# Kernel tuning notes

Hardware: AMD Instinct MI355X
Metric: run time of the kernel (lower is better)

Reference implementation:

```python
import jax, jax.numpy as jnp
import numpy as np

NUM_USERS = 100000
NUM_ITEMS = 50000
EMBED_DIM = 64
NUM_LAYERS = 3
NUM_EDGES = 1250000
N = NUM_USERS + NUM_ITEMS


def setup_inputs() -> dict:
    key = jax.random.key(0)
    k1, k2, k3 = jax.random.split(key, 3)
    edge_index = jax.random.randint(k1, (2, NUM_EDGES), 0, N, dtype=jnp.int64)
    # nn.init.normal_(std=0.1)
    user_weight = 0.1 * jax.random.normal(k2, (NUM_USERS, EMBED_DIM), dtype=jnp.float32)
    item_weight = 0.1 * jax.random.normal(k3, (NUM_ITEMS, EMBED_DIM), dtype=jnp.float32)
    return {"edge_index": edge_index, "user_weight": user_weight, "item_weight": item_weight}


def reference(edge_index, user_weight, item_weight):
    src = edge_index[0]  # [E]
    dst = edge_index[1]  # [E]
    # degrees counted from dst column only (matches the torch loop)
    deg = jax.ops.segment_sum(jnp.ones_like(src, dtype=jnp.float32), dst, num_segments=N)
    norm = 1.0 / (jnp.sqrt(deg[src]) * jnp.sqrt(deg[dst]))  # [E]
    norm = jnp.where(jnp.isfinite(norm), norm, 0.0)

    emb = jnp.concatenate([user_weight, item_weight], axis=0)  # [N, D]
    acc = emb  # running sum over layer outputs (incl. layer 0)
    cur = emb
    for _ in range(NUM_LAYERS):
        msgs = cur[src] * norm[:, None]  # [E, D]
        cur = jax.ops.segment_sum(msgs, dst, num_segments=N)
        acc = acc + cur
    all_embeddings = acc / (NUM_LAYERS + 1)
    user_embeddings = all_embeddings[:NUM_USERS]
    item_embeddings = all_embeddings[NUM_USERS:]
    return all_embeddings, user_embeddings, item_embeddings
```

## Files before the change

### kernel.cpp

```cpp
#include <hip/hip_runtime.h>


#define NU 100000
#define NI 50000
#define NN 150000
#define HALF 75000
#define DIM 64
#define NE 1250000
#define NF (NN * DIM)
#define NF4 (NF / 4)
#define SLOT 40
#define NBK 293
#define BSTRIDE 5120
#define PB 256
#define EPB ((NE + PB - 1) / PB)

typedef unsigned short ushort_t;

__device__ inline ushort_t f2bf(float f) {
    unsigned u = __float_as_uint(f);
    return (ushort_t)((u + 0x7FFF + ((u >> 16) & 1)) >> 16);
}
__device__ inline float bflo(unsigned u) { return __uint_as_float(u << 16); }
__device__ inline float bfhi(unsigned u) { return __uint_as_float(u & 0xffff0000u); }

__global__ void __launch_bounds__(1024) phaseA_kernel(const int* __restrict__ src,
                                                      const int* __restrict__ dst,
                                                      int* __restrict__ bcursor,
                                                      int* __restrict__ part) {
    __shared__ int hist[NBK];
    __shared__ int cur[NBK];
    int b = blockIdx.x;
    int tid = threadIdx.x;
    if (tid < NBK) hist[tid] = 0;
    __syncthreads();
    int e0 = b * EPB;
    int e1 = min(e0 + EPB, NE);
    for (int e = e0 + tid; e < e1; e += 1024)
        atomicAdd(&hist[dst[e] >> 9], 1);
    __syncthreads();
    if (tid < NBK) {
        int h = hist[tid];
        int base = h ? atomicAdd(&bcursor[tid], h) : 0;
        cur[tid] = tid * BSTRIDE + base;
    }
    __syncthreads();
    for (int e = e0 + tid; e < e1; e += 1024) {
        int dd = dst[e];
        int s = src[e];
        int p = atomicAdd(&cur[dd >> 9], 1);
        part[p] = ((dd & 511) << 18) | s;
    }
}

__global__ void __launch_bounds__(1024) phaseB_kernel(const int* __restrict__ bcursor,
                                                      const int* __restrict__ part,
                                                      int* __restrict__ cursor,
                                                      float* __restrict__ rdeg,
                                                      int* __restrict__ slots,
                                                      const float4* __restrict__ uw4,
                                                      const float4* __restrict__ iw4,
                                                      ushort_t* __restrict__ embb) {
    __shared__ int dcount[512];
    __shared__ float rfs[512];
    int b = blockIdx.x;
    int tid = threadIdx.x;
    int cnt = min(bcursor[b], BSTRIDE);
    int nodebase = b * 512;
    if (tid < 512) dcount[tid] = 0;
    __syncthreads();
    const int* pb = part + b * BSTRIDE;
    for (int i = tid; i < cnt; i += 1024) {
        int v = pb[i];
        int dloc = v >> 18;
        int p = atomicAdd(&dcount[dloc], 1);
        if (p < SLOT)
            slots[(nodebase + dloc) * SLOT + p] = v & 0x3FFFF;
    }
    __syncthreads();
    if (tid < 512) {
        int n = nodebase + tid;
        float r = 0.0f;
        if (n < NN) {
            int c = min(dcount[tid], SLOT);
            cursor[n] = c;
            r = (c > 0) ? rsqrtf((float)c) : 0.0f;
            rdeg[n] = r;
            int e = (c <= 8) ? 8 : ((c + 7) & ~7);
            for (int k = c; k < e; k++)
                slots[n * SLOT + k] = NN;
        }
        rfs[tid] = r;
    }
    __syncthreads();
    int nnode = min(512, NN - nodebase);
    int lim = nnode * 16;
    for (int q = tid; q < lim; q += 1024) {
        int nl = q >> 4;
        int node = nodebase + nl;
        int c4 = q & 15;
        float4 v = (node < NU) ? uw4[node * 16 + c4] : iw4[(node - NU) * 16 + c4];
        float r = rfs[nl];
        ushort4 h;
        h.x = f2bf(v.x * r); h.y = f2bf(v.y * r);
        h.z = f2bf(v.z * r); h.w = f2bf(v.w * r);
        *(ushort4*)(embb + node * DIM + c4 * 4) = h;
    }
}

template <int LAYER>
__global__ void __launch_bounds__(1024) gather_kernel(const int* __restrict__ cursor,
                                                      const float* __restrict__ rdeg,
                                                      const int* __restrict__ slots,
                                                      const ushort_t* __restrict__ cur,
                                                      const float4* __restrict__ uw4,
                                                      const float4* __restrict__ iw4,
                                                      float4* __restrict__ acc,
                                                      ushort_t* __restrict__ nxt) {
    int wid = blockIdx.x * 16 + (threadIdx.x >> 6);
    int n0 = __builtin_amdgcn_readfirstlane(wid);
    if (n0 >= HALF) return;
    int n1 = n0 + HALF;
    int lane = threadIdx.x & 63;
    int j = lane >> 4;
    int d = lane & 15;
    bool j1 = (j & 1) != 0;
    bool j2 = (j & 2) != 0;
    int dg0 = __builtin_amdgcn_readfirstlane(cursor[n0]);
    int dg1 = __builtin_amdgcn_readfirstlane(cursor[n1]);
    float rd0 = __uint_as_float(__builtin_amdgcn_readfirstlane(__float_as_uint(rdeg[n0])));
    float rd1 = __uint_as_float(__builtin_amdgcn_readfirstlane(__float_as_uint(rdeg[n1])));
    const int* sb0 = slots + n0 * SLOT;
    const int* sb1 = slots + n1 * SLOT;
    float a0 = 0, a1 = 0, a2 = 0, a3 = 0;
    float b0 = 0, b1 = 0, b2 = 0, b3 = 0;

#define GRP(SB, C, X0, X1, X2, X3)                                             \
    {                                                                          \
        int4 qa = *(const int4*)((SB) + (C));                                  \
        int4 qb = *(const int4*)((SB) + (C) + 4);                              \
        int ta = j1 ? qa.y : qa.x;                                             \
        int tb = j1 ? qa.w : qa.z;                                             \
        int sva = j2 ? tb : ta;                                                \
        int tc = j1 ? qb.y : qb.x;                                             \
        int td = j1 ? qb.w : qb.z;                                             \
        int svb = j2 ? td : tc;                                                \
        uint2 ua = *((const uint2*)(cur + sva * DIM) + d);                     \
        uint2 ub = *((const uint2*)(cur + svb * DIM) + d);                     \
        X0 += bflo(ua.x); X1 += bfhi(ua.x);                                    \
        X2 += bflo(ua.y); X3 += bfhi(ua.y);                                    \
        X0 += bflo(ub.x); X1 += bfhi(ub.x);                                    \
        X2 += bflo(ub.y); X3 += bfhi(ub.y);                                    \
    }

    GRP(sb0, 0, a0, a1, a2, a3)
    GRP(sb1, 0, b0, b1, b2, b3)
    for (int c = 8; c < dg0; c += 8) GRP(sb0, c, a0, a1, a2, a3)
    for (int c = 8; c < dg1; c += 8) GRP(sb1, c, b0, b1, b2, b3)
#undef GRP

    a0 += __shfl_xor(a0, 16); a1 += __shfl_xor(a1, 16);
    a2 += __shfl_xor(a2, 16); a3 += __shfl_xor(a3, 16);
    b0 += __shfl_xor(b0, 16); b1 += __shfl_xor(b1, 16);
    b2 += __shfl_xor(b2, 16); b3 += __shfl_xor(b3, 16);
    a0 += __shfl_xor(a0, 32); a1 += __shfl_xor(a1, 32);
    a2 += __shfl_xor(a2, 32); a3 += __shfl_xor(a3, 32);
    b0 += __shfl_xor(b0, 32); b1 += __shfl_xor(b1, 32);
    b2 += __shfl_xor(b2, 32); b3 += __shfl_xor(b3, 32);

    float c00 = rd0 * a0, c01 = rd0 * a1, c02 = rd0 * a2, c03 = rd0 * a3;
    float c10 = rd1 * b0, c11 = rd1 * b1, c12 = rd1 * b2, c13 = rd1 * b3;

    if (j == 0) {
        int i0 = n0 * 16 + d;
        int i1 = n1 * 16 + d;
        if (LAYER == 1) {
            float4 e0 = uw4[n0 * 16 + d];
            float4 e1 = (n1 < NU) ? uw4[n1 * 16 + d] : iw4[(n1 - NU) * 16 + d];
            acc[i0] = make_float4(e0.x + c00, e0.y + c01, e0.z + c02, e0.w + c03);
            acc[i1] = make_float4(e1.x + c10, e1.y + c11, e1.z + c12, e1.w + c13);
            ushort4 h0, h1;
            h0.x = f2bf(rd0 * c00); h0.y = f2bf(rd0 * c01);
            h0.z = f2bf(rd0 * c02); h0.w = f2bf(rd0 * c03);
            h1.x = f2bf(rd1 * c10); h1.y = f2bf(rd1 * c11);
            h1.z = f2bf(rd1 * c12); h1.w = f2bf(rd1 * c13);
            *(ushort4*)(nxt + n0 * DIM + d * 4) = h0;
            *(ushort4*)(nxt + n1 * DIM + d * 4) = h1;
        } else if (LAYER == 2) {
            float4 t0 = acc[i0];
            float4 t1 = acc[i1];
            acc[i0] = make_float4(t0.x + c00, t0.y + c01, t0.z + c02, t0.w + c03);
            acc[i1] = make_float4(t1.x + c10, t1.y + c11, t1.z + c12, t1.w + c13);
            ushort4 h0, h1;
            h0.x = f2bf(rd0 * c00); h0.y = f2bf(rd0 * c01);
            h0.z = f2bf(rd0 * c02); h0.w = f2bf(rd0 * c03);
            h1.x = f2bf(rd1 * c10); h1.y = f2bf(rd1 * c11);
            h1.z = f2bf(rd1 * c12); h1.w = f2bf(rd1 * c13);
            *(ushort4*)(nxt + n0 * DIM + d * 4) = h0;
            *(ushort4*)(nxt + n1 * DIM + d * 4) = h1;
        } else {
            float4 t0 = acc[i0];
            float4 t1 = acc[i1];
            float4 v0 = make_float4((t0.x + c00) * 0.25f, (t0.y + c01) * 0.25f,
                                    (t0.z + c02) * 0.25f, (t0.w + c03) * 0.25f);
            float4 v1 = make_float4((t1.x + c10) * 0.25f, (t1.y + c11) * 0.25f,
                                    (t1.z + c12) * 0.25f, (t1.w + c13) * 0.25f);
            acc[i0] = v0;
            acc[NF4 + i0] = v0;
            acc[i1] = v1;
            acc[NF4 + i1] = v1;
        }
    }
}

extern "C" void kernel_launch(void* const* d_in, const int* in_sizes, int n_in,
                              void* d_out, int out_size, void* d_ws, size_t ws_size,
                              hipStream_t stream) {
    const int* edge = (const int*)d_in[0];
    const int* src = edge;
    const int* dst = edge + NE;
    const float* uw = (const float*)d_in[1];
    const float* iw = (const float*)d_in[2];
    float* out = (float*)d_out;

    int* cursor    = (int*)d_ws;
    float* rdeg    = (float*)(cursor + NN);
    int* bcursor   = (int*)(rdeg + NN);
    int* slots     = bcursor + 320;
    int* part      = slots + NN * SLOT;
    ushort_t* embb = (ushort_t*)(part + NBK * BSTRIDE);
    ushort_t* bufA = embb;
    ushort_t* bufT = (ushort_t*)(out + NF);

    hipMemsetAsync(bcursor, 0, NBK * sizeof(int), stream);
    hipMemsetAsync(embb + NF, 0, DIM * sizeof(ushort_t), stream);
    hipMemsetAsync(bufT + NF, 0, DIM * sizeof(ushort_t), stream);

    phaseA_kernel<<<PB, 1024, 0, stream>>>(src, dst, bcursor, part);
    phaseB_kernel<<<NBK, 1024, 0, stream>>>(bcursor, part, cursor, rdeg, slots,
                                            (const float4*)uw, (const float4*)iw, embb);

    const int GB = (HALF + 15) / 16;

    gather_kernel<1><<<GB, 1024, 0, stream>>>(cursor, rdeg, slots, embb,
                                              (const float4*)uw, (const float4*)iw,
                                              (float4*)out, bufT);
    gather_kernel<2><<<GB, 1024, 0, stream>>>(cursor, rdeg, slots, bufT,
                                              (const float4*)uw, (const float4*)iw,
                                              (float4*)out, bufA);
    gather_kernel<3><<<GB, 1024, 0, stream>>>(cursor, rdeg, slots, bufA,
                                              (const float4*)uw, (const float4*)iw,
                                              (float4*)out, nullptr);
}
```

Baseline: 284.2 us.

## Compact CSR slot layout with per-node offsets and four nodes per wave

Replaces the fixed 40-slot-per-node adjacency array with a compact per-bucket CSR built by a shared-memory prefix scan in phaseB, and stores each node's offset and degree as an int2. The gather kernel now processes four nodes per wave instead of two, with each lane reading a pair of neighbor indices directly instead of selecting from int4 loads. The two memsets for the sentinel rows are folded into phaseB. This shrinks slot-array traffic and raises memory-level parallelism per wave, at the cost of more registers and a longer phaseB with extra syncs. It also drops the 40-neighbor cap, so degree handling becomes exact.

```diff
diff --git a/kernel.cpp b/kernel.cpp
--- a/kernel.cpp
+++ b/kernel.cpp
@@ -4,14 +4,14 @@
 #define NU 100000
 #define NI 50000
 #define NN 150000
-#define HALF 75000
+#define QUARTER 37500
 #define DIM 64
 #define NE 1250000
 #define NF (NN * DIM)
 #define NF4 (NF / 4)
-#define SLOT 40
 #define NBK 293
 #define BSTRIDE 5120
+#define BSLOT 8192
 #define PB 256
 #define EPB ((NE + PB - 1) / PB)
 
@@ -55,44 +55,76 @@
 
 __global__ void __launch_bounds__(1024) phaseB_kernel(const int* __restrict__ bcursor,
                                                       const int* __restrict__ part,
-                                                      int* __restrict__ cursor,
+                                                      int2* __restrict__ od,
                                                       float* __restrict__ rdeg,
                                                       int* __restrict__ slots,
                                                       const float4* __restrict__ uw4,
                                                       const float4* __restrict__ iw4,
-                                                      ushort_t* __restrict__ embb) {
+                                                      ushort_t* __restrict__ embb,
+                                                      ushort_t* __restrict__ bufT) {
+    __shared__ int stash[BSTRIDE];
     __shared__ int dcount[512];
+    __shared__ int cnt2[512];
+    __shared__ int sc[512];
+    __shared__ int offL[512];
     __shared__ float rfs[512];
     int b = blockIdx.x;
     int tid = threadIdx.x;
     int cnt = min(bcursor[b], BSTRIDE);
     int nodebase = b * 512;
     if (tid < 512) dcount[tid] = 0;
+    if (b == 0 && tid < DIM) {
+        embb[NF + tid] = 0;
+        bufT[NF + tid] = 0;
+    }
     __syncthreads();
     const int* pb = part + b * BSTRIDE;
     for (int i = tid; i < cnt; i += 1024) {
         int v = pb[i];
-        int dloc = v >> 18;
-        int p = atomicAdd(&dcount[dloc], 1);
-        if (p < SLOT)
-            slots[(nodebase + dloc) * SLOT + p] = v & 0x3FFFF;
+        stash[i] = v;
+        atomicAdd(&dcount[v >> 18], 1);
     }
     __syncthreads();
     if (tid < 512) {
+        int c = dcount[tid];
+        int pad = (c <= 8) ? 8 : ((c + 7) & ~7);
+        sc[tid] = pad;
         int n = nodebase + tid;
         float r = 0.0f;
         if (n < NN) {
-            int c = min(dcount[tid], SLOT);
-            cursor[n] = c;
             r = (c > 0) ? rsqrtf((float)c) : 0.0f;
             rdeg[n] = r;
-            int e = (c <= 8) ? 8 : ((c + 7) & ~7);
-            for (int k = c; k < e; k++)
-                slots[n * SLOT + k] = NN;
         }
         rfs[tid] = r;
     }
     __syncthreads();
+    for (int ofs = 1; ofs < 512; ofs <<= 1) {
+        int v = 0;
+        if (tid < 512 && tid >= ofs) v = sc[tid - ofs];
+        __syncthreads();
+        if (tid < 512 && tid >= ofs) sc[tid] += v;
+        __syncthreads();
+    }
+    if (tid < 512) {
+        int c = dcount[tid];
+        int pad = (c <= 8) ? 8 : ((c + 7) & ~7);
+        int off = b * BSLOT + sc[tid] - pad;
+        offL[tid] = off;
+        cnt2[tid] = 0;
+        int n = nodebase + tid;
+        if (n < NN) {
+            od[n] = make_int2(off, c);
+            for (int k = c; k < pad; k++)
+                slots[off + k] = NN;
+        }
+    }
+    __syncthreads();
+    for (int i = tid; i < cnt; i += 1024) {
+        int v = stash[i];
+        int dloc = v >> 18;
+        int p = atomicAdd(&cnt2[dloc], 1);
+        slots[offL[dloc] + p] = v & 0x3FFFF;
+    }
     int nnode = min(512, NN - nodebase);
     int lim = nnode * 16;
     for (int q = tid; q < lim; q += 1024) {
@@ -109,7 +141,7 @@
 }
 
 template <int LAYER>
-__global__ void __launch_bounds__(1024) gather_kernel(const int* __restrict__ cursor,
+__global__ void __launch_bounds__(1024) gather_kernel(const int2* __restrict__ od,
                                                       const float* __restrict__ rdeg,
                                                       const int* __restrict__ slots,
                                                       const ushort_t* __restrict__ cur,
@@ -119,98 +151,113 @@
                                                       ushort_t* __restrict__ nxt) {
     int wid = blockIdx.x * 16 + (threadIdx.x >> 6);
     int n0 = __builtin_amdgcn_readfirstlane(wid);
-    if (n0 >= HALF) return;
-    int n1 = n0 + HALF;
+    if (n0 >= QUARTER) return;
+    int n1 = n0 + QUARTER;
+    int n2 = n0 + 2 * QUARTER;
+    int n3 = n0 + 3 * QUARTER;
     int lane = threadIdx.x & 63;
-    int j = lane >> 4;
+    int j2 = (lane >> 3) & ~1;
     int d = lane & 15;
-    bool j1 = (j & 1) != 0;
-    bool j2 = (j & 2) != 0;
-    int dg0 = __builtin_amdgcn_readfirstlane(cursor[n0]);
-    int dg1 = __builtin_amdgcn_readfirstlane(cursor[n1]);
+
+    int2 v0 = od[n0];
+    int2 v1 = od[n1];
+    int2 v2 = od[n2];
+    int2 v3 = od[n3];
+    int of0 = __builtin_amdgcn_readfirstlane(v0.x);
+    int dg0 = __builtin_amdgcn_readfirstlane(v0.y);
+    int of1 = __builtin_amdgcn_readfirstlane(v1.x);
+    int dg1 = __builtin_amdgcn_readfirstlane(v1.y);
+    int of2 = __builtin_amdgcn_readfirstlane(v2.x);
+    int dg2 = __builtin_amdgcn_readfirstlane(v2.y);
+    int of3 = __builtin_amdgcn_readfirstlane(v3.x);
+    int dg3 = __builtin_amdgcn_readfirstlane(v3.y);
     float rd0 = __uint_as_float(__builtin_amdgcn_readfirstlane(__float_as_uint(rdeg[n0])));
     float rd1 = __uint_as_float(__builtin_amdgcn_readfirstlane(__float_as_uint(rdeg[n1])));
-    const int* sb0 = slots + n0 * SLOT;
-    const int* sb1 = slots + n1 * SLOT;
-    float a0 = 0, a1 = 0, a2 = 0, a3 = 0;
-    float b0 = 0, b1 = 0, b2 = 0, b3 = 0;
+    float rd2 = __uint_as_float(__builtin_amdgcn_readfirstlane(__float_as_uint(rdeg[n2])));
+    float rd3 = __uint_as_float(__builtin_amdgcn_readfirstlane(__float_as_uint(rdeg[n3])));
+    const int* sb0 = slots + of0;
+    const int* sb1 = slots + of1;
+    const int* sb2 = slots + of2;
+    const int* sb3 = slots + of3;
+    float x0 = 0, x1 = 0, x2 = 0, x3 = 0;
+    float y0 = 0, y1 = 0, y2 = 0, y3 = 0;
+    float z0 = 0, z1 = 0, z2 = 0, z3 = 0;
+    float w0 = 0, w1 = 0, w2 = 0, w3 = 0;
 
 #define GRP(SB, C, X0, X1, X2, X3)                                             \
     {                                                                          \
-        int4 qa = *(const int4*)((SB) + (C));                                  \
-        int4 qb = *(const int4*)((SB) + (C) + 4);                              \
-        int ta = j1 ? qa.y : qa.x;                                             \
-        int tb = j1 ? qa.w : qa.z;                                             \
-        int sva = j2 ? tb : ta;                                                \
-        int tc = j1 ? qb.y : qb.x;                                             \
-        int td = j1 ? qb.w : qb.z;                                             \
-        int svb = j2 ? td : tc;                                                \
-        uint2 ua = *((const uint2*)(cur + sva * DIM) + d);                     \
-        uint2 ub = *((const uint2*)(cur + svb * DIM) + d);                     \
+        int2 sv = *(const int2*)((SB) + (C) + j2);                             \
+        uint2 ua = *((const uint2*)(cur + sv.x * DIM) + d);                    \
+        uint2 ub = *((const uint2*)(cur + sv.y * DIM) + d);                    \
         X0 += bflo(ua.x); X1 += bfhi(ua.x);                                    \
         X2 += bflo(ua.y); X3 += bfhi(ua.y);                                    \
         X0 += bflo(ub.x); X1 += bfhi(ub.x);                                    \
         X2 += bflo(ub.y); X3 += bfhi(ub.y);                                    \
     }
 
-    GRP(sb0, 0, a0, a1, a2, a3)
-    GRP(sb1, 0, b0, b1, b2, b3)
-    for (int c = 8; c < dg0; c += 8) GRP(sb0, c, a0, a1, a2, a3)
-    for (int c = 8; c < dg1; c += 8) GRP(sb1, c, b0, b1, b2, b3)
+    GRP(sb0, 0, x0, x1, x2, x3)
+    GRP(sb1, 0, y0, y1, y2, y3)
+    GRP(sb2, 0, z0, z1, z2, z3)
+    GRP(sb3, 0, w0, w1, w2, w3)
+    for (int c = 8; c < dg0; c += 8) GRP(sb0, c, x0, x1, x2, x3)
+    for (int c = 8; c < dg1; c += 8) GRP(sb1, c, y0, y1, y2, y3)
+    for (int c = 8; c < dg2; c += 8) GRP(sb2, c, z0, z1, z2, z3)
+    for (int c = 8; c < dg3; c += 8) GRP(sb3, c, w0, w1, w2, w3)
 #undef GRP
 
-    a0 += __shfl_xor(a0, 16); a1 += __shfl_xor(a1, 16);
-    a2 += __shfl_xor(a2, 16); a3 += __shfl_xor(a3, 16);
-    b0 += __shfl_xor(b0, 16); b1 += __shfl_xor(b1, 16);
-    b2 += __shfl_xor(b2, 16); b3 += __shfl_xor(b3, 16);
-    a0 += __shfl_xor(a0, 32); a1 += __shfl_xor(a1, 32);
-    a2 += __shfl_xor(a2, 32); a3 += __shfl_xor(a3, 32);
-    b0 += __shfl_xor(b0, 32); b1 += __shfl_xor(b1, 32);
-    b2 += __shfl_xor(b2, 32); b3 += __shfl_xor(b3, 32);
-
-    float c00 = rd0 * a0, c01 = rd0 * a1, c02 = rd0 * a2, c03 = rd0 * a3;
-    float c10 = rd1 * b0, c11 = rd1 * b1, c12 = rd1 * b2, c13 = rd1 * b3;
-
-    if (j == 0) {
-        int i0 = n0 * 16 + d;
-        int i1 = n1 * 16 + d;
-        if (LAYER == 1) {
-            float4 e0 = uw4[n0 * 16 + d];
-            float4 e1 = (n1 < NU) ? uw4[n1 * 16 + d] : iw4[(n1 - NU) * 16 + d];
-            acc[i0] = make_float4(e0.x + c00, e0.y + c01, e0.z + c02, e0.w + c03);
-            acc[i1] = make_float4(e1.x + c10, e1.y + c11, e1.z + c12, e1.w + c13);
-            ushort4 h0, h1;
-            h0.x = f2bf(rd0 * c00); h0.y = f2bf(rd0 * c01);
-            h0.z = f2bf(rd0 * c02); h0.w = f2bf(rd0 * c03);
-            h1.x = f2bf(rd1 * c10); h1.y = f2bf(rd1 * c11);
-            h1.z = f2bf(rd1 * c12); h1.w = f2bf(rd1 * c13);
-            *(ushort4*)(nxt + n0 * DIM + d * 4) = h0;
-            *(ushort4*)(nxt + n1 * DIM + d * 4) = h1;
-        } else if (LAYER == 2) {
-            float4 t0 = acc[i0];
-            float4 t1 = acc[i1];
-            acc[i0] = make_float4(t0.x + c00, t0.y + c01, t0.z + c02, t0.w + c03);
-            acc[i1] = make_float4(t1.x + c10, t1.y + c11, t1.z + c12, t1.w + c13);
-            ushort4 h0, h1;
-            h0.x = f2bf(rd0 * c00); h0.y = f2bf(rd0 * c01);
-            h0.z = f2bf(rd0 * c02); h0.w = f2bf(rd0 * c03);
-            h1.x = f2bf(rd1 * c10); h1.y = f2bf(rd1 * c11);
-            h1.z = f2bf(rd1 * c12); h1.w = f2bf(rd1 * c13);
-            *(ushort4*)(nxt + n0 * DIM + d * 4) = h0;
-            *(ushort4*)(nxt + n1 * DIM + d * 4) = h1;
-        } else {
-            float4 t0 = acc[i0];
-            float4 t1 = acc[i1];
-            float4 v0 = make_float4((t0.x + c00) * 0.25f, (t0.y + c01) * 0.25f,
-                                    (t0.z + c02) * 0.25f, (t0.w + c03) * 0.25f);
-            float4 v1 = make_float4((t1.x + c10) * 0.25f, (t1.y + c11) * 0.25f,
-                                    (t1.z + c12) * 0.25f, (t1.w + c13) * 0.25f);
-            acc[i0] = v0;
-            acc[NF4 + i0] = v0;
-            acc[i1] = v1;
-            acc[NF4 + i1] = v1;
-        }
-    }
+    x0 += __shfl_xor(x0, 16); x1 += __shfl_xor(x1, 16);
+    x2 += __shfl_xor(x2, 16); x3 += __shfl_xor(x3, 16);
+    y0 += __shfl_xor(y0, 16); y1 += __shfl_xor(y1, 16);
+    y2 += __shfl_xor(y2, 16); y3 += __shfl_xor(y3, 16);
+    z0 += __shfl_xor(z0, 16); z1 += __shfl_xor(z1, 16);
+    z2 += __shfl_xor(z2, 16); z3 += __shfl_xor(z3, 16);
+    w0 += __shfl_xor(w0, 16); w1 += __shfl_xor(w1, 16);
+    w2 += __shfl_xor(w2, 16); w3 += __shfl_xor(w3, 16);
+    x0 += __shfl_xor(x0, 32); x1 += __shfl_xor(x1, 32);
+    x2 += __shfl_xor(x2, 32); x3 += __shfl_xor(x3, 32);
+    y0 += __shfl_xor(y0, 32); y1 += __shfl_xor(y1, 32);
+    y2 += __shfl_xor(y2, 32); y3 += __shfl_xor(y3, 32);
+    z0 += __shfl_xor(z0, 32); z1 += __shfl_xor(z1, 32);
+    z2 += __shfl_xor(z2, 32); z3 += __shfl_xor(z3, 32);
+    w0 += __shfl_xor(w0, 32); w1 += __shfl_xor(w1, 32);
+    w2 += __shfl_xor(w2, 32); w3 += __shfl_xor(w3, 32);
+
+    if ((lane >> 4) != 0) return;
+
+#define EPI(N, RD, A0, A1, A2, A3, EMB)                                        \
+    {                                                                          \
+        float c0 = (RD) * (A0), c1 = (RD) * (A1);                              \
+        float c2 = (RD) * (A2), c3 = (RD) * (A3);                              \
+        int i4 = (N) * 16 + d;                                                 \
+        if (LAYER == 1) {                                                      \
+            float4 e = (EMB);                                                  \
+            acc[i4] = make_float4(e.x + c0, e.y + c1, e.z + c2, e.w + c3);     \
+            ushort4 h;                                                         \
+            h.x = f2bf((RD) * c0); h.y = f2bf((RD) * c1);                      \
+            h.z = f2bf((RD) * c2); h.w = f2bf((RD) * c3);                      \
+            *(ushort4*)(nxt + (N) * DIM + d * 4) = h;                          \
+        } else if (LAYER == 2) {                                               \
+            float4 t = acc[i4];                                                \
+            acc[i4] = make_float4(t.x + c0, t.y + c1, t.z + c2, t.w + c3);     \
+            ushort4 h;                                                         \
+            h.x = f2bf((RD) * c0); h.y = f2bf((RD) * c1);                      \
+            h.z = f2bf((RD) * c2); h.w = f2bf((RD) * c3);                      \
+            *(ushort4*)(nxt + (N) * DIM + d * 4) = h;                          \
+        } else {                                                               \
+            float4 t = acc[i4];                                                \
+            float4 v = make_float4((t.x + c0) * 0.25f, (t.y + c1) * 0.25f,     \
+                                   (t.z + c2) * 0.25f, (t.w + c3) * 0.25f);    \
+            acc[i4] = v;                                                       \
+            acc[NF4 + i4] = v;                                                 \
+        }                                                                      \
+    }
+
+    EPI(n0, rd0, x0, x1, x2, x3, uw4[n0 * 16 + d])
+    EPI(n1, rd1, y0, y1, y2, y3, uw4[n1 * 16 + d])
+    EPI(n2, rd2, z0, z1, z2, z3,
+        ((n2 < NU) ? uw4[n2 * 16 + d] : iw4[(n2 - NU) * 16 + d]))
+    EPI(n3, rd3, w0, w1, w2, w3, iw4[(n3 - NU) * 16 + d])
+#undef EPI
 }
 
 extern "C" void kernel_launch(void* const* d_in, const int* in_sizes, int n_in,
@@ -223,32 +270,31 @@
     const float* iw = (const float*)d_in[2];
     float* out = (float*)d_out;
 
-    int* cursor    = (int*)d_ws;
-    float* rdeg    = (float*)(cursor + NN);
+    int2* od       = (int2*)d_ws;
+    float* rdeg    = (float*)(od + NN);
     int* bcursor   = (int*)(rdeg + NN);
     int* slots     = bcursor + 320;
-    int* part      = slots + NN * SLOT;
+    int* part      = slots + NBK * BSLOT;
     ushort_t* embb = (ushort_t*)(part + NBK * BSTRIDE);
     ushort_t* bufA = embb;
     ushort_t* bufT = (ushort_t*)(out + NF);
 
     hipMemsetAsync(bcursor, 0, NBK * sizeof(int), stream);
-    hipMemsetAsync(embb + NF, 0, DIM * sizeof(ushort_t), stream);
-    hipMemsetAsync(bufT + NF, 0, DIM * sizeof(ushort_t), stream);
 
     phaseA_kernel<<<PB, 1024, 0, stream>>>(src, dst, bcursor, part);
-    phaseB_kernel<<<NBK, 1024, 0, stream>>>(bcursor, part, cursor, rdeg, slots,
-                                            (const float4*)uw, (const float4*)iw, embb);
-
-    const int GB = (HALF + 15) / 16;
-
-    gather_kernel<1><<<GB, 1024, 0, stream>>>(cursor, rdeg, slots, embb,
+    phaseB_kernel<<<NBK, 1024, 0, stream>>>(bcursor, part, od, rdeg, slots,
+                                            (const float4*)uw, (const float4*)iw,
+                                            embb, bufT);
+
+    const int GB = (QUARTER + 15) / 16;
+
+    gather_kernel<1><<<GB, 1024, 0, stream>>>(od, rdeg, slots, embb,
                                               (const float4*)uw, (const float4*)iw,
                                               (float4*)out, bufT);
-    gather_kernel<2><<<GB, 1024, 0, stream>>>(cursor, rdeg, slots, bufT,
+    gather_kernel<2><<<GB, 1024, 0, stream>>>(od, rdeg, slots, bufT,
                                               (const float4*)uw, (const float4*)iw,
                                               (float4*)out, bufA);
-    gather_kernel<3><<<GB, 1024, 0, stream>>>(cursor, rdeg, slots, bufA,
+    gather_kernel<3><<<GB, 1024, 0, stream>>>(od, rdeg, slots, bufA,
                                               (const float4*)uw, (const float4*)iw,
                                               (float4*)out, nullptr);
 }
```

After: 318.2 us. 12.0% more time.

## Replace fixed-slot adjacency with compact CSR-like per-bucket packed slots

Applied to the files above, without the earlier changes.

Phase B now stashes each bucket's edges in shared memory, counts degrees, and runs a prefix scan over padded counts. It then writes neighbour lists contiguously per bucket instead of into fixed 40-entry slots per node, and stores offset and degree packed in one word. The gather kernel recomputes rsqrt from the degree, so it drops the separate cursor and rdeg loads. This shrinks the adjacency footprint and improves locality of slot reads, and it also removes the 40-neighbour truncation. Two small memsets are folded into the kernel, at the cost of extra shared memory and barriers in phase B.

```diff
diff --git a/kernel.cpp b/kernel.cpp
--- a/kernel.cpp
+++ b/kernel.cpp
@@ -9,9 +9,9 @@
 #define NE 1250000
 #define NF (NN * DIM)
 #define NF4 (NF / 4)
-#define SLOT 40
 #define NBK 293
 #define BSTRIDE 5120
+#define BSLOT 8192
 #define PB 256
 #define EPB ((NE + PB - 1) / PB)
 
@@ -55,44 +55,69 @@
 
 __global__ void __launch_bounds__(1024) phaseB_kernel(const int* __restrict__ bcursor,
                                                       const int* __restrict__ part,
-                                                      int* __restrict__ cursor,
-                                                      float* __restrict__ rdeg,
+                                                      unsigned* __restrict__ od,
                                                       int* __restrict__ slots,
                                                       const float4* __restrict__ uw4,
                                                       const float4* __restrict__ iw4,
-                                                      ushort_t* __restrict__ embb) {
+                                                      ushort_t* __restrict__ embb,
+                                                      ushort_t* __restrict__ bufT) {
+    __shared__ int stash[BSTRIDE];
     __shared__ int dcount[512];
+    __shared__ int cnt2[512];
+    __shared__ int sc[512];
+    __shared__ int offL[512];
     __shared__ float rfs[512];
     int b = blockIdx.x;
     int tid = threadIdx.x;
     int cnt = min(bcursor[b], BSTRIDE);
     int nodebase = b * 512;
     if (tid < 512) dcount[tid] = 0;
+    if (b == 0 && tid < DIM) {
+        embb[NF + tid] = 0;
+        bufT[NF + tid] = 0;
+    }
     __syncthreads();
     const int* pb = part + b * BSTRIDE;
     for (int i = tid; i < cnt; i += 1024) {
         int v = pb[i];
+        stash[i] = v;
+        atomicAdd(&dcount[v >> 18], 1);
+    }
+    __syncthreads();
+    if (tid < 512) {
+        int c = dcount[tid];
+        int pad = (c <= 8) ? 8 : ((c + 7) & ~7);
+        sc[tid] = pad;
+        rfs[tid] = (c > 0) ? rsqrtf((float)c) : 0.0f;
+    }
+    __syncthreads();
+    for (int ofs = 1; ofs < 512; ofs <<= 1) {
+        int v = 0;
+        if (tid < 512 && tid >= ofs) v = sc[tid - ofs];
+        __syncthreads();
+        if (tid < 512 && tid >= ofs) sc[tid] += v;
+        __syncthreads();
+    }
+    if (tid < 512) {
+        int c = dcount[tid];
+        int pad = (c <= 8) ? 8 : ((c + 7) & ~7);
+        int off = b * BSLOT + sc[tid] - pad;
+        offL[tid] = off;
+        cnt2[tid] = 0;
+        int n = nodebase + tid;
+        if (n < NN) {
+            od[n] = (unsigned)off | ((unsigned)c << 26);
+            for (int k = c; k < pad; k++)
+                slots[off + k] = NN;
+        }
+    }
+    __syncthreads();
+    for (int i = tid; i < cnt; i += 1024) {
+        int v = stash[i];
         int dloc = v >> 18;
-        int p = atomicAdd(&dcount[dloc], 1);
-        if (p < SLOT)
-            slots[(nodebase + dloc) * SLOT + p] = v & 0x3FFFF;
-    }
-    __syncthreads();
-    if (tid < 512) {
-        int n = nodebase + tid;
-        float r = 0.0f;
-        if (n < NN) {
-            int c = min(dcount[tid], SLOT);
-            cursor[n] = c;
-            r = (c > 0) ? rsqrtf((float)c) : 0.0f;
-            rdeg[n] = r;
-            int e = (c <= 8) ? 8 : ((c + 7) & ~7);
-            for (int k = c; k < e; k++)
-                slots[n * SLOT + k] = NN;
-        }
-        rfs[tid] = r;
-    }
-    __syncthreads();
+        int p = atomicAdd(&cnt2[dloc], 1);
+        slots[offL[dloc] + p] = v & 0x3FFFF;
+    }
     int nnode = min(512, NN - nodebase);
     int lim = nnode * 16;
     for (int q = tid; q < lim; q += 1024) {
@@ -109,8 +134,7 @@
 }
 
 template <int LAYER>
-__global__ void __launch_bounds__(1024) gather_kernel(const int* __restrict__ cursor,
-                                                      const float* __restrict__ rdeg,
+__global__ void __launch_bounds__(1024) gather_kernel(const unsigned* __restrict__ od,
                                                       const int* __restrict__ slots,
                                                       const ushort_t* __restrict__ cur,
                                                       const float4* __restrict__ uw4,
@@ -126,12 +150,16 @@
     int d = lane & 15;
     bool j1 = (j & 1) != 0;
     bool j2 = (j & 2) != 0;
-    int dg0 = __builtin_amdgcn_readfirstlane(cursor[n0]);
-    int dg1 = __builtin_amdgcn_readfirstlane(cursor[n1]);
-    float rd0 = __uint_as_float(__builtin_amdgcn_readfirstlane(__float_as_uint(rdeg[n0])));
-    float rd1 = __uint_as_float(__builtin_amdgcn_readfirstlane(__float_as_uint(rdeg[n1])));
-    const int* sb0 = slots + n0 * SLOT;
-    const int* sb1 = slots + n1 * SLOT;
+    unsigned v0 = (unsigned)__builtin_amdgcn_readfirstlane((int)od[n0]);
+    unsigned v1 = (unsigned)__builtin_amdgcn_readfirstlane((int)od[n1]);
+    int of0 = (int)(v0 & 0x3FFFFFFu);
+    int dg0 = (int)(v0 >> 26);
+    int of1 = (int)(v1 & 0x3FFFFFFu);
+    int dg1 = (int)(v1 >> 26);
+    float rd0 = (dg0 > 0) ? rsqrtf((float)dg0) : 0.0f;
+    float rd1 = (dg1 > 0) ? rsqrtf((float)dg1) : 0.0f;
+    const int* sb0 = slots + of0;
+    const int* sb1 = slots + of1;
     float a0 = 0, a1 = 0, a2 = 0, a3 = 0;
     float b0 = 0, b1 = 0, b2 = 0, b3 = 0;
 
@@ -223,32 +251,30 @@
     const float* iw = (const float*)d_in[2];
     float* out = (float*)d_out;
 
-    int* cursor    = (int*)d_ws;
-    float* rdeg    = (float*)(cursor + NN);
-    int* bcursor   = (int*)(rdeg + NN);
+    unsigned* od   = (unsigned*)d_ws;
+    int* bcursor   = (int*)(od + NN);
     int* slots     = bcursor + 320;
-    int* part      = slots + NN * SLOT;
+    int* part      = slots + NBK * BSLOT;
     ushort_t* embb = (ushort_t*)(part + NBK * BSTRIDE);
     ushort_t* bufA = embb;
     ushort_t* bufT = (ushort_t*)(out + NF);
 
     hipMemsetAsync(bcursor, 0, NBK * sizeof(int), stream);
-    hipMemsetAsync(embb + NF, 0, DIM * sizeof(ushort_t), stream);
-    hipMemsetAsync(bufT + NF, 0, DIM * sizeof(ushort_t), stream);
 
     phaseA_kernel<<<PB, 1024, 0, stream>>>(src, dst, bcursor, part);
-    phaseB_kernel<<<NBK, 1024, 0, stream>>>(bcursor, part, cursor, rdeg, slots,
-                                            (const float4*)uw, (const float4*)iw, embb);
+    phaseB_kernel<<<NBK, 1024, 0, stream>>>(bcursor, part, od, slots,
+                                            (const float4*)uw, (const float4*)iw,
+                                            embb, bufT);
 
     const int GB = (HALF + 15) / 16;
 
-    gather_kernel<1><<<GB, 1024, 0, stream>>>(cursor, rdeg, slots, embb,
+    gather_kernel<1><<<GB, 1024, 0, stream>>>(od, slots, embb,
                                               (const float4*)uw, (const float4*)iw,
                                               (float4*)out, bufT);
-    gather_kernel<2><<<GB, 1024, 0, stream>>>(cursor, rdeg, slots, bufT,
+    gather_kernel<2><<<GB, 1024, 0, stream>>>(od, slots, bufT,
                                               (const float4*)uw, (const float4*)iw,
                                               (float4*)out, bufA);
-    gather_kernel<3><<<GB, 1024, 0, stream>>>(cursor, rdeg, slots, bufA,
+    gather_kernel<3><<<GB, 1024, 0, stream>>>(od, slots, bufA,
                                               (const float4*)uw, (const float4*)iw,
                                               (float4*)out, nullptr);
 }
```

Measured after the change: 307.2 us. +8.1%, slower.

## Fuse three gather layers into a persistent kernel with LDS accumulators

Applied to the files above, without the earlier changes.

The three per-layer gather launches become one persistent kernel of 256 blocks. Each block owns 586 nodes, keeps their fp32 running sums in shared memory, and separates layers with a software grid barrier. This removes the global-memory read-modify-write of the accumulator and two kernel launches. In exchange, occupancy drops to 16 waves per CU for a latency-bound gather, and the barrier assumes every block is resident at once. Separately, the partition kernel now stages packed edges in shared memory so src and dst are read only once, and it uses twice as many blocks.

```diff
diff --git a/kernel.cpp b/kernel.cpp
--- a/kernel.cpp
+++ b/kernel.cpp
@@ -4,7 +4,6 @@
 #define NU 100000
 #define NI 50000
 #define NN 150000
-#define HALF 75000
 #define DIM 64
 #define NE 1250000
 #define NF (NN * DIM)
@@ -12,8 +11,11 @@
 #define SLOT 40
 #define NBK 293
 #define BSTRIDE 5120
-#define PB 256
-#define EPB ((NE + PB - 1) / PB)
+#define PB 512
+#define EPB 2442
+#define GRID 256
+#define NPB 586
+#define PAIRS 293
 
 typedef unsigned short ushort_t;
 
@@ -30,14 +32,23 @@
                                                       int* __restrict__ part) {
     __shared__ int hist[NBK];
     __shared__ int cur[NBK];
+    __shared__ int pk[EPB];
+    __shared__ short bk[EPB];
     int b = blockIdx.x;
     int tid = threadIdx.x;
     if (tid < NBK) hist[tid] = 0;
     __syncthreads();
     int e0 = b * EPB;
     int e1 = min(e0 + EPB, NE);
-    for (int e = e0 + tid; e < e1; e += 1024)
-        atomicAdd(&hist[dst[e] >> 9], 1);
+    int cnt = e1 - e0;
+    for (int k = tid; k < cnt; k += 1024) {
+        int dd = dst[e0 + k];
+        int s = src[e0 + k];
+        int bb = dd >> 9;
+        pk[k] = ((dd & 511) << 18) | s;
+        bk[k] = (short)bb;
+        atomicAdd(&hist[bb], 1);
+    }
     __syncthreads();
     if (tid < NBK) {
         int h = hist[tid];
@@ -45,11 +56,9 @@
         cur[tid] = tid * BSTRIDE + base;
     }
     __syncthreads();
-    for (int e = e0 + tid; e < e1; e += 1024) {
-        int dd = dst[e];
-        int s = src[e];
-        int p = atomicAdd(&cur[dd >> 9], 1);
-        part[p] = ((dd & 511) << 18) | s;
+    for (int k = tid; k < cnt; k += 1024) {
+        int p = atomicAdd(&cur[(int)bk[k]], 1);
+        part[p] = pk[k];
     }
 }
 
@@ -108,32 +117,72 @@
     }
 }
 
-template <int LAYER>
-__global__ void __launch_bounds__(1024) gather_kernel(const int* __restrict__ cursor,
-                                                      const float* __restrict__ rdeg,
-                                                      const int* __restrict__ slots,
-                                                      const ushort_t* __restrict__ cur,
-                                                      const float4* __restrict__ uw4,
-                                                      const float4* __restrict__ iw4,
-                                                      float4* __restrict__ acc,
-                                                      ushort_t* __restrict__ nxt) {
-    int wid = blockIdx.x * 16 + (threadIdx.x >> 6);
-    int n0 = __builtin_amdgcn_readfirstlane(wid);
-    if (n0 >= HALF) return;
-    int n1 = n0 + HALF;
-    int lane = threadIdx.x & 63;
+__device__ inline void gsync(int* cnt, int* gen, int target) {
+    __syncthreads();
+    if (threadIdx.x == 0) {
+        __threadfence();
+        if (atomicAdd(cnt, 1) == GRID - 1) {
+            atomicExch(cnt, 0);
+            __threadfence();
+            atomicExch(gen, target);
+        } else {
+            while (atomicAdd(gen, 0) < target)
+                __builtin_amdgcn_s_sleep(8);
+        }
+        __threadfence();
+    }
+    __syncthreads();
+}
+
+__global__ void __launch_bounds__(1024) fused_kernel(const int* __restrict__ cursor,
+                                                     const float* __restrict__ rdeg,
+                                                     const int* __restrict__ slots,
+                                                     const ushort_t* __restrict__ p0,
+                                                     ushort_t* __restrict__ p1,
+                                                     ushort_t* __restrict__ p2,
+                                                     const float4* __restrict__ uw4,
+                                                     const float4* __restrict__ iw4,
+                                                     float4* __restrict__ outv,
+                                                     int* __restrict__ bar_cnt,
+                                                     int* __restrict__ bar_gen) {
+    __shared__ float accL[NPB * DIM];
+    float4* acc4 = (float4*)accL;
+    int blk = blockIdx.x;
+    int base = blk * NPB;
+    int tid = threadIdx.x;
+    int nloc = min(NPB, NN - base);
+
+    for (int q = tid; q < nloc * 16; q += 1024) {
+        int n = base + (q >> 4);
+        acc4[q] = (n < NU) ? uw4[n * 16 + (q & 15)] : iw4[(n - NU) * 16 + (q & 15)];
+    }
+    __syncthreads();
+
+    int wv = tid >> 6;
+    int lane = tid & 63;
     int j = lane >> 4;
     int d = lane & 15;
     bool j1 = (j & 1) != 0;
     bool j2 = (j & 2) != 0;
-    int dg0 = __builtin_amdgcn_readfirstlane(cursor[n0]);
-    int dg1 = __builtin_amdgcn_readfirstlane(cursor[n1]);
-    float rd0 = __uint_as_float(__builtin_amdgcn_readfirstlane(__float_as_uint(rdeg[n0])));
-    float rd1 = __uint_as_float(__builtin_amdgcn_readfirstlane(__float_as_uint(rdeg[n1])));
-    const int* sb0 = slots + n0 * SLOT;
-    const int* sb1 = slots + n1 * SLOT;
-    float a0 = 0, a1 = 0, a2 = 0, a3 = 0;
-    float b0 = 0, b1 = 0, b2 = 0, b3 = 0;
+
+    for (int L = 0; L < 3; ++L) {
+        const ushort_t* cur = (L == 0) ? p0 : (L == 1) ? p1 : p2;
+        ushort_t* nxt = (L == 0) ? p1 : (L == 1) ? p2 : nullptr;
+
+        for (int i = wv; i < PAIRS; i += 16) {
+            int l0 = i;
+            int l1 = i + PAIRS;
+            bool has1 = (l1 < nloc);
+            int n0 = base + l0;
+            int n1 = base + (has1 ? l1 : 0);
+            int dg0 = __builtin_amdgcn_readfirstlane(cursor[n0]);
+            int dg1 = has1 ? __builtin_amdgcn_readfirstlane(cursor[n1]) : 0;
+            float rd0 = __uint_as_float(__builtin_amdgcn_readfirstlane(__float_as_uint(rdeg[n0])));
+            float rd1 = has1 ? __uint_as_float(__builtin_amdgcn_readfirstlane(__float_as_uint(rdeg[n1]))) : 0.0f;
+            const int* sb0 = slots + n0 * SLOT;
+            const int* sb1 = slots + n1 * SLOT;
+            float a0 = 0, a1 = 0, a2 = 0, a3 = 0;
+            float b0 = 0, b1 = 0, b2 = 0, b3 = 0;
 
 #define GRP(SB, C, X0, X1, X2, X3)                                             \
     {                                                                          \
@@ -152,64 +201,57 @@
         X0 += bflo(ub.x); X1 += bfhi(ub.x);                                    \
         X2 += bflo(ub.y); X3 += bfhi(ub.y);                                    \
     }
-
-    GRP(sb0, 0, a0, a1, a2, a3)
-    GRP(sb1, 0, b0, b1, b2, b3)
-    for (int c = 8; c < dg0; c += 8) GRP(sb0, c, a0, a1, a2, a3)
-    for (int c = 8; c < dg1; c += 8) GRP(sb1, c, b0, b1, b2, b3)
+            GRP(sb0, 0, a0, a1, a2, a3)
+            GRP(sb1, 0, b0, b1, b2, b3)
+            for (int c = 8; c < dg0; c += 8) GRP(sb0, c, a0, a1, a2, a3)
+            for (int c = 8; c < dg1; c += 8) GRP(sb1, c, b0, b1, b2, b3)
 #undef GRP
 
-    a0 += __shfl_xor(a0, 16); a1 += __shfl_xor(a1, 16);
-    a2 += __shfl_xor(a2, 16); a3 += __shfl_xor(a3, 16);
-    b0 += __shfl_xor(b0, 16); b1 += __shfl_xor(b1, 16);
-    b2 += __shfl_xor(b2, 16); b3 += __shfl_xor(b3, 16);
-    a0 += __shfl_xor(a0, 32); a1 += __shfl_xor(a1, 32);
-    a2 += __shfl_xor(a2, 32); a3 += __shfl_xor(a3, 32);
-    b0 += __shfl_xor(b0, 32); b1 += __shfl_xor(b1, 32);
-    b2 += __shfl_xor(b2, 32); b3 += __shfl_xor(b3, 32);
-
-    float c00 = rd0 * a0, c01 = rd0 * a1, c02 = rd0 * a2, c03 = rd0 * a3;
-    float c10 = rd1 * b0, c11 = rd1 * b1, c12 = rd1 * b2, c13 = rd1 * b3;
-
-    if (j == 0) {
-        int i0 = n0 * 16 + d;
-        int i1 = n1 * 16 + d;
-        if (LAYER == 1) {
-            float4 e0 = uw4[n0 * 16 + d];
-            float4 e1 = (n1 < NU) ? uw4[n1 * 16 + d] : iw4[(n1 - NU) * 16 + d];
-            acc[i0] = make_float4(e0.x + c00, e0.y + c01, e0.z + c02, e0.w + c03);
-            acc[i1] = make_float4(e1.x + c10, e1.y + c11, e1.z + c12, e1.w + c13);
-            ushort4 h0, h1;
-            h0.x = f2bf(rd0 * c00); h0.y = f2bf(rd0 * c01);
-            h0.z = f2bf(rd0 * c02); h0.w = f2bf(rd0 * c03);
-            h1.x = f2bf(rd1 * c10); h1.y = f2bf(rd1 * c11);
-            h1.z = f2bf(rd1 * c12); h1.w = f2bf(rd1 * c13);
-            *(ushort4*)(nxt + n0 * DIM + d * 4) = h0;
-            *(ushort4*)(nxt + n1 * DIM + d * 4) = h1;
-        } else if (LAYER == 2) {
-            float4 t0 = acc[i0];
-            float4 t1 = acc[i1];
-            acc[i0] = make_float4(t0.x + c00, t0.y + c01, t0.z + c02, t0.w + c03);
-            acc[i1] = make_float4(t1.x + c10, t1.y + c11, t1.z + c12, t1.w + c13);
-            ushort4 h0, h1;
-            h0.x = f2bf(rd0 * c00); h0.y = f2bf(rd0 * c01);
-            h0.z = f2bf(rd0 * c02); h0.w = f2bf(rd0 * c03);
-            h1.x = f2bf(rd1 * c10); h1.y = f2bf(rd1 * c11);
-            h1.z = f2bf(rd1 * c12); h1.w = f2bf(rd1 * c13);
-            *(ushort4*)(nxt + n0 * DIM + d * 4) = h0;
-            *(ushort4*)(nxt + n1 * DIM + d * 4) = h1;
-        } else {
-            float4 t0 = acc[i0];
-            float4 t1 = acc[i1];
-            float4 v0 = make_float4((t0.x + c00) * 0.25f, (t0.y + c01) * 0.25f,
-                                    (t0.z + c02) * 0.25f, (t0.w + c03) * 0.25f);
-            float4 v1 = make_float4((t1.x + c10) * 0.25f, (t1.y + c11) * 0.25f,
-                                    (t1.z + c12) * 0.25f, (t1.w + c13) * 0.25f);
-            acc[i0] = v0;
-            acc[NF4 + i0] = v0;
-            acc[i1] = v1;
-            acc[NF4 + i1] = v1;
+            a0 += __shfl_xor(a0, 16); a1 += __shfl_xor(a1, 16);
+            a2 += __shfl_xor(a2, 16); a3 += __shfl_xor(a3, 16);
+            b0 += __shfl_xor(b0, 16); b1 += __shfl_xor(b1, 16);
+            b2 += __shfl_xor(b2, 16); b3 += __shfl_xor(b3, 16);
+            a0 += __shfl_xor(a0, 32); a1 += __shfl_xor(a1, 32);
+            a2 += __shfl_xor(a2, 32); a3 += __shfl_xor(a3, 32);
+            b0 += __shfl_xor(b0, 32); b1 += __shfl_xor(b1, 32);
+            b2 += __shfl_xor(b2, 32); b3 += __shfl_xor(b3, 32);
+
+            float c00 = rd0 * a0, c01 = rd0 * a1, c02 = rd0 * a2, c03 = rd0 * a3;
+            float c10 = rd1 * b0, c11 = rd1 * b1, c12 = rd1 * b2, c13 = rd1 * b3;
+
+            if (j == 0) {
+                float4* ap0 = acc4 + l0 * 16 + d;
+                float4 t0 = *ap0;
+                *ap0 = make_float4(t0.x + c00, t0.y + c01, t0.z + c02, t0.w + c03);
+                if (nxt) {
+                    ushort4 h0;
+                    h0.x = f2bf(rd0 * c00); h0.y = f2bf(rd0 * c01);
+                    h0.z = f2bf(rd0 * c02); h0.w = f2bf(rd0 * c03);
+                    *(ushort4*)(nxt + n0 * DIM + d * 4) = h0;
+                }
+                if (has1) {
+                    float4* ap1 = acc4 + l1 * 16 + d;
+                    float4 t1 = *ap1;
+                    *ap1 = make_float4(t1.x + c10, t1.y + c11, t1.z + c12, t1.w + c13);
+                    if (nxt) {
+                        ushort4 h1;
+                        h1.x = f2bf(rd1 * c10); h1.y = f2bf(rd1 * c11);
+                        h1.z = f2bf(rd1 * c12); h1.w = f2bf(rd1 * c13);
+                        *(ushort4*)(nxt + n1 * DIM + d * 4) = h1;
+                    }
+                }
+            }
         }
+        if (L < 2) gsync(bar_cnt, bar_gen, L + 1);
+    }
+    __syncthreads();
+
+    for (int q = tid; q < nloc * 16; q += 1024) {
+        float4 v = acc4[q];
+        v = make_float4(v.x * 0.25f, v.y * 0.25f, v.z * 0.25f, v.w * 0.25f);
+        int n = base + (q >> 4);
+        outv[n * 16 + (q & 15)] = v;
+        outv[NF4 + n * 16 + (q & 15)] = v;
     }
 }
 
@@ -231,8 +273,10 @@
     ushort_t* embb = (ushort_t*)(part + NBK * BSTRIDE);
     ushort_t* bufA = embb;
     ushort_t* bufT = (ushort_t*)(out + NF);
+    int* bar       = (int*)(embb + NF + DIM);
 
     hipMemsetAsync(bcursor, 0, NBK * sizeof(int), stream);
+    hipMemsetAsync(bar, 0, 2 * sizeof(int), stream);
     hipMemsetAsync(embb + NF, 0, DIM * sizeof(ushort_t), stream);
     hipMemsetAsync(bufT + NF, 0, DIM * sizeof(ushort_t), stream);
 
@@ -240,15 +284,7 @@
     phaseB_kernel<<<NBK, 1024, 0, stream>>>(bcursor, part, cursor, rdeg, slots,
                                             (const float4*)uw, (const float4*)iw, embb);
 
-    const int GB = (HALF + 15) / 16;
-
-    gather_kernel<1><<<GB, 1024, 0, stream>>>(cursor, rdeg, slots, embb,
-                                              (const float4*)uw, (const float4*)iw,
-                                              (float4*)out, bufT);
-    gather_kernel<2><<<GB, 1024, 0, stream>>>(cursor, rdeg, slots, bufT,
-                                              (const float4*)uw, (const float4*)iw,
-                                              (float4*)out, bufA);
-    gather_kernel<3><<<GB, 1024, 0, stream>>>(cursor, rdeg, slots, bufA,
-                                              (const float4*)uw, (const float4*)iw,
-                                              (float4*)out, nullptr);
-}
+    fused_kernel<<<GRID, 1024, 0, stream>>>(cursor, rdeg, slots, embb, bufT, bufA,
+                                            (const float4*)uw, (const float4*)iw,
+                                            (float4*)out, bar, bar + 1);
+}
```

New measurement: 400.1 us. +40.8%, slower.
